# Optimization experiments

Hardware: AMD Instinct MI355X
Metric: run time of the kernel (lower is better)

## Reference

```python
import jax, jax.numpy as jnp
import numpy as np

IN_SIZE = 1024
OUT_SIZE = 3 * IN_SIZE  # must equal 3*in_size for trigger_a * attn broadcast
B, S = 32, 512


def setup_inputs() -> dict:
    key = jax.random.key(0)
    ks = jax.random.split(key, 8)
    h_state = jax.random.normal(ks[0], (B, S, 2 * IN_SIZE), dtype=jnp.float32)
    x = jax.random.normal(ks[1], (B, S, IN_SIZE), dtype=jnp.float32)
    trigger = jax.random.randint(ks[2], (B,), 0, S)
    mask = jax.random.randint(ks[3], (B, S), 0, 2).astype(jnp.int32)
    # learned params (nn.Linear: y = x @ W.T + b; store pre-transposed as (in, out))
    Wa = jax.random.normal(ks[4], (3 * IN_SIZE, OUT_SIZE), dtype=jnp.float32) / np.sqrt(3 * IN_SIZE)
    ba = jnp.zeros((OUT_SIZE,), dtype=jnp.float32)
    Ws = jax.random.normal(ks[5], (2 * IN_SIZE, OUT_SIZE), dtype=jnp.float32) / np.sqrt(2 * IN_SIZE)
    bs = jnp.zeros((OUT_SIZE,), dtype=jnp.float32)
    return {"h_state": h_state, "x": x, "trigger": trigger, "mask": mask,
            "Wa": Wa, "ba": ba, "Ws": Ws, "bs": bs}


def reference(h_state, x, trigger, mask, Wa, ba, Ws, bs):
    # a: (B, S, 3*in_size)
    a = jnp.concatenate([h_state, x], axis=-1)
    b = a.shape[0]
    # one_hot + masked_select in the original == gather of the trigger row per batch
    trigger_a = a[jnp.arange(b), trigger]  # (B, 3*in_size)
    s = h_state.sum(axis=1)  # (B, 2*in_size)
    # et: (B, S, out_size)
    et = jnp.tanh(a @ Wa + ba + (s @ Ws + bs)[:, None, :])
    # masked_fill where mask == 0 (mask broadcast over feature dim)
    et = jnp.where(mask[:, :, None] == 0, jnp.float32(-1e9), et)
    # softmax over the FEATURE dim (dim=-1), as in the original; dropout in eval mode is identity
    attn = jax.nn.softmax(et, axis=-1)
    # trigger-weighted reduction over the sequence dim
    out = (trigger_a[:, None, :] * attn).sum(axis=1)  # (B, out_size)
    return out
```

## Files before the change

kernel.cpp:

```cpp
#include <hip/hip_runtime.h>
#include <hip/hip_bf16.h>
#include <hip/hip_fp16.h>


namespace {
constexpr int SIN  = 1024;
constexpr int KH   = 2048;
constexpr int NF   = 3072;
constexpr int NBAT = 32;
constexpr int NS   = 512;
constexpr int NM   = NBAT * NS;
constexpr int NDB  = NF / 64;
constexpr int KC   = 8;
constexpr int NKT  = NF / 64;
constexpr int NCH  = 8;
}

typedef unsigned short u16;
typedef __bf16 bf16x8 __attribute__((ext_vector_type(8)));
typedef float  f32x4  __attribute__((ext_vector_type(4)));

#define ASYNC_CP16(gptr, lptr)                                                              \
  __builtin_amdgcn_global_load_lds((__attribute__((address_space(1))) void*)(gptr),         \
                                   (__attribute__((address_space(3))) void*)(lptr), 16, 0, 0)

__device__ __forceinline__ u16 f2b(float f) {
  union { float f; unsigned u; } v; v.f = f;
  unsigned u = v.u;
  u += 0x7FFFu + ((u >> 16) & 1u);
  return (u16)(u >> 16);
}

__global__ __launch_bounds__(64) void k_cnt(const int* __restrict__ mask,
                                            int* __restrict__ bcnt) {
  int b = blockIdx.x, t = threadIdx.x;
  int c = 0;
#pragma unroll
  for (int i = 0; i < NS / 64; ++i) c += mask[b * NS + i * 64 + t];
#pragma unroll
  for (int off = 32; off >= 1; off >>= 1) c += __shfl_down(c, off, 64);
  if (t == 0) bcnt[b] = c;
}

__global__ __launch_bounds__(64) void k_scan(const int* __restrict__ bcnt,
                                             int* __restrict__ boff,
                                             int* __restrict__ meta) {
  if (threadIdx.x == 0) {
    int run = 0;
    for (int b = 0; b < NBAT; ++b) { boff[b] = run; run += bcnt[b]; }
    meta[0] = run;
    meta[1] = (run + 255) & ~255;
  }
}

__global__ __launch_bounds__(512) void k_gather(const int* __restrict__ mask,
                                                const int* __restrict__ boff,
                                                const int* __restrict__ meta,
                                                int* __restrict__ rowmap) {
  __shared__ int ps[NS];
  int b = blockIdx.x, t = threadIdx.x;
  int m = mask[b * NS + t];
  ps[t] = m;
  __syncthreads();
#pragma unroll
  for (int off = 1; off < NS; off <<= 1) {
    int v = (t >= off) ? ps[t - off] : 0;
    __syncthreads();
    ps[t] += v;
    __syncthreads();
  }
  if (m) rowmap[boff[b] + ps[t] - m] = b * NS + t;
  if (b == 0) {
    int Mc = meta[0], McPad = meta[1];
    if (Mc + t < McPad) rowmap[Mc + t] = 0;
  }
}

__global__ __launch_bounds__(256) void k_sum_h(const float* __restrict__ h,
                                               float* __restrict__ s) {
  int b = blockIdx.x;
  int d = blockIdx.y * 256 + threadIdx.x;
  const float* p = h + (size_t)b * NS * KH + d;
  float acc = 0.f;
#pragma unroll 8
  for (int t = 0; t < NS; ++t) acc += p[(size_t)t * KH];
  s[b * KH + d] = acc;
}

__global__ __launch_bounds__(256) void k_base1(const float* __restrict__ s,
                                               const float* __restrict__ Ws,
                                               float* __restrict__ basep) {
  __shared__ float sT[NBAT][KH / KC];
  int f  = blockIdx.x * 256 + threadIdx.x;
  int k0 = blockIdx.y * (KH / KC);
  for (int it = 0; it < NBAT; ++it) {
    int idx = it * 256 + threadIdx.x;
    int b = idx >> 8, kk = idx & 255;
    sT[b][kk] = s[b * KH + k0 + kk];
  }
  __syncthreads();
  float acc[NBAT] = {};
  for (int k = 0; k < KH / KC; ++k) {
    float w = Ws[(size_t)(k0 + k) * NF + f];
#pragma unroll
    for (int b = 0; b < NBAT; ++b) acc[b] += sT[b][k] * w;
  }
#pragma unroll
  for (int b = 0; b < NBAT; ++b)
    basep[((size_t)blockIdx.y * NBAT + b) * NF + f] = acc[b];
}

__global__ __launch_bounds__(256) void k_base2(const float* __restrict__ basep,
                                               const float* __restrict__ ba,
                                               const float* __restrict__ bs,
                                               float* __restrict__ base) {
  int b = blockIdx.x;
  int f = blockIdx.y * 256 + threadIdx.x;
  float acc = 0.f;
#pragma unroll
  for (int kc = 0; kc < KC; ++kc) acc += basep[((size_t)kc * NBAT + b) * NF + f];
  base[b * NF + f] = acc + ba[f] + bs[f];
}

__global__ __launch_bounds__(256) void k_cvt_a(const float* __restrict__ h,
                                               const float* __restrict__ x,
                                               const int* __restrict__ rowmap,
                                               const int* __restrict__ meta,
                                               u16* __restrict__ A) {
  int tid = blockIdx.x * 256 + threadIdx.x;
  int i = tid / (NF / 4);
  if (i >= meta[1]) return;
  int k = (tid - i * (NF / 4)) * 4;
  ushort4 o;
  if (i >= meta[0]) {
    o.x = o.y = o.z = o.w = 0;
  } else {
    int ro = rowmap[i];
    int b = ro >> 9, t = ro & 511;
    const float* src = (k < KH) ? h + ((size_t)b * NS + t) * KH + k
                                : x + ((size_t)b * NS + t) * SIN + (k - KH);
    float4 v = *(const float4*)src;
    o.x = f2b(v.x); o.y = f2b(v.y); o.z = f2b(v.z); o.w = f2b(v.w);
  }
  *(ushort4*)(A + (size_t)i * NF + k) = o;
}

__global__ __launch_bounds__(256) void k_wat(const float* __restrict__ Wa,
                                             u16* __restrict__ WaT) {
  __shared__ float tile[64][65];
  int k0 = blockIdx.x * 64, f0 = blockIdx.y * 64;
  int tid = threadIdx.x;
  int col4 = (tid & 15) * 4, row = tid >> 4;
#pragma unroll
  for (int rr = 0; rr < 64; rr += 16) {
    float4 v = *(const float4*)(Wa + (size_t)(k0 + row + rr) * NF + f0 + col4);
    tile[row + rr][col4 + 0] = v.x; tile[row + rr][col4 + 1] = v.y;
    tile[row + rr][col4 + 2] = v.z; tile[row + rr][col4 + 3] = v.w;
  }
  __syncthreads();
#pragma unroll
  for (int rr = 0; rr < 64; rr += 16) {
    int f = f0 + row + rr;
    ushort4 o;
    o.x = f2b(tile[col4 + 0][row + rr]); o.y = f2b(tile[col4 + 1][row + rr]);
    o.z = f2b(tile[col4 + 2][row + rr]); o.w = f2b(tile[col4 + 3][row + rr]);
    *(ushort4*)(WaT + (size_t)f * NF + k0 + col4) = o;
  }
}

#define LDSOFF(row, gg) ((row) * 32 + ((((gg) ^ (((row) >> 1) & 3))) << 3))

#define LDB4(BUF, KS)                                                        \
  _Pragma("unroll") for (int nf = 0; nf < 4; ++nf) {                         \
    int rb = wc * 64 + nf * 16 + lr;                                         \
    bfr[nf] = *(const bf16x8*)&lds[BUF][1][KS][LDSOFF(rb, g)];               \
  }

#define LDA4(BUF, KS, MH)                                                    \
  _Pragma("unroll") for (int mf = 0; mf < 4; ++mf) {                         \
    int ra = wr * 128 + ((MH) * 4 + mf) * 16 + lr;                           \
    afr[mf] = *(const bf16x8*)&lds[BUF][0][KS][LDSOFF(ra, g)];               \
  }

#define MFMA16(MH)                                                           \
  _Pragma("unroll") for (int mf = 0; mf < 4; ++mf)                           \
  _Pragma("unroll") for (int nf = 0; nf < 4; ++nf)                           \
    acc[(MH) * 4 + mf][nf] = __builtin_amdgcn_mfma_f32_16x16x32_bf16(        \
        afr[mf], bfr[nf], acc[(MH) * 4 + mf][nf], 0, 0, 0);

#define STAGE(SMAT, SBUF, SKS, SKT)                                          \
  if ((SKT) < NKT) {                                                         \
    _Pragma("unroll") for (int q = 0; q < 2; ++q) {                          \
      const u16* src = ((SMAT) ? pB[q] : pA[q]) + (SKT) * 64 + (SKS) * 32;   \
      ASYNC_CP16(src, &lds[SBUF][SMAT][SKS][q * 4096 + wid * 512]);          \
    }                                                                        \
  }

#define PH(BUF, KS, MH, SMAT, SBUF, SKS, SKT)                                \
  {                                                                          \
    if ((MH) == 0) { LDB4(BUF, KS) }                                         \
    LDA4(BUF, KS, MH)                                                        \
    STAGE(SMAT, SBUF, SKS, SKT)                                              \
    __builtin_amdgcn_s_setprio(1);                                           \
    MFMA16(MH)                                                               \
    __builtin_amdgcn_s_setprio(0);                                           \
    asm volatile("s_waitcnt vmcnt(6)" ::: "memory");                         \
    __builtin_amdgcn_s_barrier();                                            \
  }

__global__ __launch_bounds__(512, 2) void k_gemm(const u16* __restrict__ A,
                                                 const u16* __restrict__ Wt,
                                                 const float* __restrict__ base,
                                                 const int* __restrict__ rowmap,
                                                 const int* __restrict__ meta,
                                                 __half* __restrict__ P,
                                                 float* __restrict__ Dpart) {
  __shared__ __align__(16) u16 lds[2][2][2][8192];
  const int MT   = meta[1] >> 8;
  const int nact = MT * 12;
  const int flat = blockIdx.x;
  if (flat >= nact) return;
  const int qx = nact >> 3, rx = nact & 7;
  const int xcd = flat & 7, idx = flat >> 3;
  const int swz = (xcd < rx) ? xcd * (qx + 1) + idx
                             : rx * (qx + 1) + (xcd - rx) * qx + idx;
  const int mt = swz / 12, nt = swz - mt * 12;
  const int r0 = mt << 8, c0 = nt << 8;

  const int tid = threadIdx.x;
  const int wid = tid >> 6, lane = tid & 63;
  const int wr = wid >> 2, wc = wid & 3;
  const int g = lane >> 4, lr = lane & 15;

  const u16* pA[2]; const u16* pB[2];
#pragma unroll
  for (int q = 0; q < 2; ++q) {
    int c = q * 512 + tid;
    int row = c >> 2;
    int kc8 = (((c & 3) ^ ((row >> 1) & 3)) << 3);
    pA[q] = A  + (size_t)(r0 + row) * NF + kc8;
    pB[q] = Wt + (size_t)(c0 + row) * NF + kc8;
  }

  f32x4 acc[8][4] = {};
  bf16x8 afr[4], bfr[4];

  STAGE(0, 0, 0, 0) STAGE(1, 0, 0, 0)
  STAGE(0, 0, 1, 0) STAGE(1, 0, 1, 0)
  STAGE(0, 1, 0, 1) STAGE(1, 1, 0, 1)
  asm volatile("s_waitcnt vmcnt(8)" ::: "memory");
  __builtin_amdgcn_s_barrier();

#pragma unroll 1
  for (int i = 0; i < NKT / 2; ++i) {
    const int kt1 = 2 * i + 1, kt2 = 2 * i + 2, kt3 = 2 * i + 3;
    PH(0, 0, 0, 0, 1, 1, kt1)
    PH(0, 0, 1, 1, 1, 1, kt1)
    PH(0, 1, 0, 0, 0, 0, kt2)
    PH(0, 1, 1, 1, 0, 0, kt2)
    PH(1, 0, 0, 0, 0, 1, kt2)
    PH(1, 0, 1, 1, 0, 1, kt2)
    PH(1, 1, 0, 0, 1, 0, kt3)
    PH(1, 1, 1, 1, 1, 0, kt3)
  }

  const int cbase = c0 + wc * 64;
#pragma unroll
  for (int mf = 0; mf < 8; ++mf) {
#pragma unroll
    for (int j = 0; j < 4; ++j) {
      int i = r0 + wr * 128 + mf * 16 + g * 4 + j;
      int b = rowmap[i] >> 9;
      float rs = 0.f;
#pragma unroll
      for (int nf = 0; nf < 4; ++nf) {
        int ccn = cbase + nf * 16 + lr;
        float z  = acc[mf][nf][j] + base[b * NF + ccn];
        z        = fminf(fmaxf(z, -15.f), 15.f);
        float e2 = __expf(2.f * z);
        float th = (e2 - 1.f) / (e2 + 1.f);
        float p  = __expf(th);
        P[(size_t)i * NF + ccn] = __float2half(p);
        rs += p;
      }
#pragma unroll
      for (int off = 1; off < 16; off <<= 1) rs += __shfl_xor(rs, off, 64);
      if (lr == 0) Dpart[(size_t)i * NDB + (cbase >> 6)] = rs;
    }
  }
}

__global__ __launch_bounds__(256) void k_invd(const float* __restrict__ Dpart,
                                              const int* __restrict__ meta,
                                              float* __restrict__ invD) {
  int i = blockIdx.x * 256 + threadIdx.x;
  if (i >= meta[1]) return;
  float d = 0.f;
#pragma unroll
  for (int q = 0; q < NDB; ++q) d += Dpart[(size_t)i * NDB + q];
  invD[i] = 1.0f / d;
}

__global__ __launch_bounds__(256) void k_final1(const __half* __restrict__ P,
                                                const float* __restrict__ invD,
                                                const int* __restrict__ boff,
                                                const int* __restrict__ bcnt,
                                                float* __restrict__ pb) {
  int c = blockIdx.x;
  int b = c >> 3, j = c & 7;
  int f = blockIdx.y * 256 + threadIdx.x;
  int cnt = bcnt[b];
  int lo = j * 64, hi = min(cnt, lo + 64);
  int off = boff[b];
  float acc = 0.f;
  for (int t = lo; t < hi; ++t)
    acc += __half2float(P[(size_t)(off + t) * NF + f]) * invD[off + t];
  pb[(size_t)c * NF + f] = acc;
}

__global__ __launch_bounds__(256) void k_final2(const float* __restrict__ pb,
                                                const int* __restrict__ bcnt,
                                                const float* __restrict__ h,
                                                const float* __restrict__ x,
                                                const int* __restrict__ trig,
                                                float* __restrict__ out) {
  int b = blockIdx.x;
  int f = blockIdx.y * 256 + threadIdx.x;
  float acc = 0.f;
#pragma unroll
  for (int j = 0; j < NCH; ++j) acc += pb[(size_t)(b * NCH + j) * NF + f];
  acc += (float)(NS - bcnt[b]) * (1.0f / (float)NF);
  int tr = trig[b];
  float ta = (f < KH) ? h[((size_t)b * NS + tr) * KH + f]
                      : x[((size_t)b * NS + tr) * SIN + f - KH];
  out[b * NF + f] = acc * ta;
}

extern "C" void kernel_launch(void* const* d_in, const int* in_sizes, int n_in,
                              void* d_out, int out_size, void* d_ws, size_t ws_size,
                              hipStream_t stream) {
  const float* h_state = (const float*)d_in[0];
  const float* x       = (const float*)d_in[1];
  const int*   trigger = (const int*)d_in[2];
  const int*   mask    = (const int*)d_in[3];
  const float* Wa      = (const float*)d_in[4];
  const float* ba      = (const float*)d_in[5];
  const float* Ws      = (const float*)d_in[6];
  const float* bs      = (const float*)d_in[7];
  float*       out     = (float*)d_out;

  char* w = (char*)d_ws;
  u16*    Abf   = (u16*)w;                 w += (size_t)NM * NF * 2;
  u16*    WaT   = (u16*)w;                 w += (size_t)NF * NF * 2;
  __half* P     = (__half*)w;              w += (size_t)NM * NF * 2;
  float*  s     = (float*)w;               w += (size_t)NBAT * KH * 4;
  float*  base  = (float*)w;               w += (size_t)NBAT * NF * 4;
  float*  Dpart = (float*)w;               w += (size_t)NM * NDB * 4;
  float*  basep = (float*)Dpart;
  float*  pb    = (float*)Dpart;
  float*  invD  = (float*)w;               w += (size_t)NM * 4;
  int*    rowmap= (int*)w;                 w += (size_t)NM * 4;
  int*    bcnt  = (int*)w;                 w += 128;
  int*    boff  = (int*)w;                 w += 128;
  int*    meta  = (int*)w;                 w += 128;

  (void)in_sizes; (void)n_in; (void)out_size; (void)ws_size;

  k_cnt   <<<dim3(NBAT), 64, 0, stream>>>(mask, bcnt);
  k_scan  <<<dim3(1), 64, 0, stream>>>(bcnt, boff, meta);
  k_gather<<<dim3(NBAT), 512, 0, stream>>>(mask, boff, meta, rowmap);
  k_sum_h <<<dim3(NBAT, KH / 256), 256, 0, stream>>>(h_state, s);
  k_cvt_a <<<dim3(NM * (NF / 4) / 256), 256, 0, stream>>>(h_state, x, rowmap, meta, Abf);
  k_wat   <<<dim3(NF / 64, NF / 64), 256, 0, stream>>>(Wa, WaT);
  k_base1 <<<dim3(NF / 256, KC), 256, 0, stream>>>(s, Ws, basep);
  k_base2 <<<dim3(NBAT, NF / 256), 256, 0, stream>>>(basep, ba, bs, base);
  k_gemm  <<<dim3((NF / 256) * (NM / 256)), 512, 0, stream>>>(Abf, WaT, base, rowmap, meta, P, Dpart);
  k_invd  <<<dim3(NM / 256), 256, 0, stream>>>(Dpart, meta, invD);
  k_final1<<<dim3(NBAT * NCH, NF / 256), 256, 0, stream>>>(P, invD, boff, bcnt, pb);
  k_final2<<<dim3(NBAT, NF / 256), 256, 0, stream>>>(pb, bcnt, h_state, x, trigger, out);
}
```

Before: 417.0 us.

## Retile GEMM to 256x192 with single-stage B buffer and vectorize final reduction

Changes the GEMM output tile from 256x256 to 256x192. B now uses a single 64-wide K stage per buffer with a new XOR swizzle, and the async-copy staging schedule and vmcnt waits are reworked to match. This gives 16 column tiles and more blocks, which should fill the CUs better, and the partial-denominator layout is resized to 64 slots. Separately, k_final1 now handles two features per thread with half2 loads and caches invD in shared memory. The smaller tile lowers MFMA reuse per loaded A byte, and the hand-tuned pipeline waits are easy to get wrong.

```diff
diff --git a/kernel.cpp b/kernel.cpp
--- a/kernel.cpp
+++ b/kernel.cpp
@@ -10,7 +10,7 @@
 constexpr int NBAT = 32;
 constexpr int NS   = 512;
 constexpr int NM   = NBAT * NS;
-constexpr int NDB  = NF / 64;
+constexpr int NDB  = 64;
 constexpr int KC   = 8;
 constexpr int NKT  = NF / 64;
 constexpr int NCH  = 8;
@@ -170,41 +170,43 @@
 
 #define LDSOFF(row, gg) ((row) * 32 + ((((gg) ^ (((row) >> 1) & 3))) << 3))
 
-#define LDB4(BUF, KS)                                                        \
-  _Pragma("unroll") for (int nf = 0; nf < 4; ++nf) {                         \
-    int rb = wc * 64 + nf * 16 + lr;                                         \
-    bfr[nf] = *(const bf16x8*)&lds[BUF][1][KS][LDSOFF(rb, g)];               \
+#define LDB3(BUF, KS)                                                        \
+  _Pragma("unroll") for (int nf = 0; nf < 3; ++nf) {                         \
+    int rb = wc * 48 + nf * 16 + lr;                                         \
+    bfr[nf] = *(const bf16x8*)                                               \
+        &ldsB[BUF][rb * 64 + (((((KS) * 4) + g) ^ (rb & 7)) << 3)];          \
   }
 
 #define LDA4(BUF, KS, MH)                                                    \
   _Pragma("unroll") for (int mf = 0; mf < 4; ++mf) {                         \
     int ra = wr * 128 + ((MH) * 4 + mf) * 16 + lr;                           \
-    afr[mf] = *(const bf16x8*)&lds[BUF][0][KS][LDSOFF(ra, g)];               \
-  }
-
-#define MFMA16(MH)                                                           \
+    afr[mf] = *(const bf16x8*)&ldsA[BUF][KS][LDSOFF(ra, g)];                 \
+  }
+
+#define MFMA12(MH)                                                           \
   _Pragma("unroll") for (int mf = 0; mf < 4; ++mf)                           \
-  _Pragma("unroll") for (int nf = 0; nf < 4; ++nf)                           \
+  _Pragma("unroll") for (int nf = 0; nf < 3; ++nf)                           \
     acc[(MH) * 4 + mf][nf] = __builtin_amdgcn_mfma_f32_16x16x32_bf16(        \
         afr[mf], bfr[nf], acc[(MH) * 4 + mf][nf], 0, 0, 0);
 
-#define STAGE(SMAT, SBUF, SKS, SKT)                                          \
-  if ((SKT) < NKT) {                                                         \
-    _Pragma("unroll") for (int q = 0; q < 2; ++q) {                          \
-      const u16* src = ((SMAT) ? pB[q] : pA[q]) + (SKT) * 64 + (SKS) * 32;   \
-      ASYNC_CP16(src, &lds[SBUF][SMAT][SKS][q * 4096 + wid * 512]);          \
-    }                                                                        \
-  }
-
-#define PH(BUF, KS, MH, SMAT, SBUF, SKS, SKT)                                \
+#define STAGE_A(SBUF, SKS, Q, SKT)                                           \
+  if ((SKT) < NKT)                                                           \
+    ASYNC_CP16(pA[Q] + (SKT) * 64 + (SKS) * 32,                              \
+               &ldsA[SBUF][SKS][(Q) * 4096 + wid * 512]);
+
+#define STAGE_B(SBUF, Q, SKT)                                                \
+  if ((SKT) < NKT)                                                           \
+    ASYNC_CP16(pBg[Q] + (SKT) * 64, &ldsB[SBUF][(Q) * 4096 + wid * 512]);
+
+#define PH(BUF, KS, MH, VM, STAGES)                                          \
   {                                                                          \
-    if ((MH) == 0) { LDB4(BUF, KS) }                                         \
+    if ((MH) == 0) { LDB3(BUF, KS) }                                         \
     LDA4(BUF, KS, MH)                                                        \
-    STAGE(SMAT, SBUF, SKS, SKT)                                              \
+    STAGES                                                                   \
     __builtin_amdgcn_s_setprio(1);                                           \
-    MFMA16(MH)                                                               \
+    MFMA12(MH)                                                               \
     __builtin_amdgcn_s_setprio(0);                                           \
-    asm volatile("s_waitcnt vmcnt(6)" ::: "memory");                         \
+    if (VM) asm volatile("s_waitcnt vmcnt(3)" ::: "memory");                 \
     __builtin_amdgcn_s_barrier();                                            \
   }
 
@@ -215,56 +217,66 @@
                                                  const int* __restrict__ meta,
                                                  __half* __restrict__ P,
                                                  float* __restrict__ Dpart) {
-  __shared__ __align__(16) u16 lds[2][2][2][8192];
+  __shared__ __align__(16) u16 ldsA[2][2][8192];
+  __shared__ __align__(16) u16 ldsB[2][12288];
   const int MT   = meta[1] >> 8;
-  const int nact = MT * 12;
+  const int nact = MT * 16;
   const int flat = blockIdx.x;
   if (flat >= nact) return;
   const int qx = nact >> 3, rx = nact & 7;
   const int xcd = flat & 7, idx = flat >> 3;
   const int swz = (xcd < rx) ? xcd * (qx + 1) + idx
                              : rx * (qx + 1) + (xcd - rx) * qx + idx;
-  const int mt = swz / 12, nt = swz - mt * 12;
-  const int r0 = mt << 8, c0 = nt << 8;
+  const int mt = swz >> 4, nt = swz & 15;
+  const int r0 = mt << 8, c0 = nt * 192;
 
   const int tid = threadIdx.x;
   const int wid = tid >> 6, lane = tid & 63;
   const int wr = wid >> 2, wc = wid & 3;
   const int g = lane >> 4, lr = lane & 15;
 
-  const u16* pA[2]; const u16* pB[2];
+  const u16* pA[2];
 #pragma unroll
   for (int q = 0; q < 2; ++q) {
     int c = q * 512 + tid;
     int row = c >> 2;
     int kc8 = (((c & 3) ^ ((row >> 1) & 3)) << 3);
-    pA[q] = A  + (size_t)(r0 + row) * NF + kc8;
-    pB[q] = Wt + (size_t)(c0 + row) * NF + kc8;
-  }
-
-  f32x4 acc[8][4] = {};
-  bf16x8 afr[4], bfr[4];
-
-  STAGE(0, 0, 0, 0) STAGE(1, 0, 0, 0)
-  STAGE(0, 0, 1, 0) STAGE(1, 0, 1, 0)
-  STAGE(0, 1, 0, 1) STAGE(1, 1, 0, 1)
-  asm volatile("s_waitcnt vmcnt(8)" ::: "memory");
+    pA[q] = A + (size_t)(r0 + row) * NF + kc8;
+  }
+  const u16* pBg[3];
+#pragma unroll
+  for (int q = 0; q < 3; ++q) {
+    int row = q * 64 + (tid >> 3);
+    int cz = (((tid & 7) ^ ((tid >> 3) & 7)) << 3);
+    pBg[q] = Wt + (size_t)(c0 + row) * NF + cz;
+  }
+
+  f32x4 acc[8][3] = {};
+  bf16x8 afr[4], bfr[3];
+
+  STAGE_A(0, 0, 0, 0) STAGE_A(0, 0, 1, 0)
+  STAGE_A(0, 1, 0, 0) STAGE_A(0, 1, 1, 0)
+  STAGE_B(0, 0, 0)    STAGE_B(0, 1, 0)    STAGE_B(0, 2, 0)
+  STAGE_A(1, 0, 0, 1) STAGE_A(1, 0, 1, 1)
+  STAGE_B(1, 0, 1)
+  asm volatile("s_waitcnt vmcnt(3)" ::: "memory");
   __builtin_amdgcn_s_barrier();
 
 #pragma unroll 1
   for (int i = 0; i < NKT / 2; ++i) {
-    const int kt1 = 2 * i + 1, kt2 = 2 * i + 2, kt3 = 2 * i + 3;
-    PH(0, 0, 0, 0, 1, 1, kt1)
-    PH(0, 0, 1, 1, 1, 1, kt1)
-    PH(0, 1, 0, 0, 0, 0, kt2)
-    PH(0, 1, 1, 1, 0, 0, kt2)
-    PH(1, 0, 0, 0, 0, 1, kt2)
-    PH(1, 0, 1, 1, 0, 1, kt2)
-    PH(1, 1, 0, 0, 1, 0, kt3)
-    PH(1, 1, 1, 1, 1, 0, kt3)
-  }
-
-  const int cbase = c0 + wc * 64;
+    const int kto = 2 * i + 1, kt2 = 2 * i + 2, kt3 = 2 * i + 3;
+    PH(0, 0, 0, 0, STAGE_A(1, 1, 0, kto) STAGE_A(1, 1, 1, kto))
+    PH(0, 0, 1, 0, STAGE_B(1, 1, kto)    STAGE_B(1, 2, kto))
+    PH(0, 1, 0, 0, STAGE_A(0, 0, 0, kt2) STAGE_A(0, 0, 1, kt2))
+    PH(0, 1, 1, 1, STAGE_B(0, 0, kt2))
+    PH(1, 0, 0, 0, STAGE_B(0, 1, kt2)    STAGE_A(0, 1, 0, kt2))
+    PH(1, 0, 1, 0, STAGE_B(0, 2, kt2)    STAGE_A(0, 1, 1, kt2))
+    PH(1, 1, 0, 0, STAGE_A(1, 0, 0, kt3) STAGE_A(1, 0, 1, kt3))
+    PH(1, 1, 1, 1, STAGE_B(1, 0, kt3))
+  }
+
+  const int cbase = c0 + wc * 48;
+  const int dcol  = nt * 4 + wc;
 #pragma unroll
   for (int mf = 0; mf < 8; ++mf) {
 #pragma unroll
@@ -273,7 +285,7 @@
       int b = rowmap[i] >> 9;
       float rs = 0.f;
 #pragma unroll
-      for (int nf = 0; nf < 4; ++nf) {
+      for (int nf = 0; nf < 3; ++nf) {
         int ccn = cbase + nf * 16 + lr;
         float z  = acc[mf][nf][j] + base[b * NF + ccn];
         z        = fminf(fmaxf(z, -15.f), 15.f);
@@ -285,7 +297,7 @@
       }
 #pragma unroll
       for (int off = 1; off < 16; off <<= 1) rs += __shfl_xor(rs, off, 64);
-      if (lr == 0) Dpart[(size_t)i * NDB + (cbase >> 6)] = rs;
+      if (lr == 0) Dpart[(size_t)i * NDB + dcol] = rs;
     }
   }
 }
@@ -308,14 +320,23 @@
                                                 float* __restrict__ pb) {
   int c = blockIdx.x;
   int b = c >> 3, j = c & 7;
-  int f = blockIdx.y * 256 + threadIdx.x;
+  int f = blockIdx.y * 512 + threadIdx.x * 2;
   int cnt = bcnt[b];
   int lo = j * 64, hi = min(cnt, lo + 64);
   int off = boff[b];
-  float acc = 0.f;
-  for (int t = lo; t < hi; ++t)
-    acc += __half2float(P[(size_t)(off + t) * NF + f]) * invD[off + t];
-  pb[(size_t)c * NF + f] = acc;
+  __shared__ float ivs[64];
+  if (threadIdx.x < 64 && lo + (int)threadIdx.x < hi)
+    ivs[threadIdx.x] = invD[off + lo + threadIdx.x];
+  __syncthreads();
+  float ax = 0.f, ay = 0.f;
+  for (int t = lo; t < hi; ++t) {
+    __half2 hv = *(const __half2*)(P + (size_t)(off + t) * NF + f);
+    float2 fv = __half22float2(hv);
+    float iv = ivs[t - lo];
+    ax += fv.x * iv; ay += fv.y * iv;
+  }
+  float2 o; o.x = ax; o.y = ay;
+  *(float2*)(pb + (size_t)c * NF + f) = o;
 }
 
 __global__ __launch_bounds__(256) void k_final2(const float* __restrict__ pb,
@@ -374,8 +395,8 @@
   k_wat   <<<dim3(NF / 64, NF / 64), 256, 0, stream>>>(Wa, WaT);
   k_base1 <<<dim3(NF / 256, KC), 256, 0, stream>>>(s, Ws, basep);
   k_base2 <<<dim3(NBAT, NF / 256), 256, 0, stream>>>(basep, ba, bs, base);
-  k_gemm  <<<dim3((NF / 256) * (NM / 256)), 512, 0, stream>>>(Abf, WaT, base, rowmap, meta, P, Dpart);
+  k_gemm  <<<dim3((NF / 192) * (NM / 256)), 512, 0, stream>>>(Abf, WaT, base, rowmap, meta, P, Dpart);
   k_invd  <<<dim3(NM / 256), 256, 0, stream>>>(Dpart, meta, invD);
-  k_final1<<<dim3(NBAT * NCH, NF / 256), 256, 0, stream>>>(P, invD, boff, bcnt, pb);
+  k_final1<<<dim3(NBAT * NCH, NF / 512), 256, 0, stream>>>(P, invD, boff, bcnt, pb);
   k_final2<<<dim3(NBAT, NF / 256), 256, 0, stream>>>(pb, bcnt, h_state, x, trigger, out);
 }
```

New measurement: 468.1 us. 12.2% more time.
